# Performance work log

Hardware: AMD Instinct MI355X
Metric: run time of the kernel (lower is better)

Reference implementation:

```python
import jax, jax.numpy as jnp
import numpy as np

N = 50000   # nodes
E = 1600000 # edges
F = 128     # node feature dim
D_ENC, D_EMB, D_H = 32, 12, 128
TEMPERATURE = 10.0


def _dense(key, fan_in, fan_out):
    kw, kb = jax.random.split(key)
    W = jax.random.normal(kw, (fan_in, fan_out), jnp.float32) * (1.0 / jnp.sqrt(fan_in))
    b = jnp.zeros((fan_out,), jnp.float32)
    return W, b


def setup_inputs() -> dict:
    key = jax.random.key(0)
    ks = jax.random.split(key, 12)
    nodes = jax.random.normal(ks[0], (N, F), jnp.float32)
    senders = jax.random.randint(ks[1], (E,), 0, N, dtype=jnp.int32)
    receivers = jax.random.randint(ks[2], (E,), 0, N, dtype=jnp.int32)
    W_enc, b_enc = _dense(ks[3], F, D_ENC)
    W_inf, b_inf = _dense(ks[4], D_ENC + 1, 1)
    W_emb, b_emb = _dense(ks[5], F, D_EMB)
    W1, b1 = _dense(ks[6], D_EMB, D_H)
    W2, b2 = _dense(ks[7], D_H, D_H)
    Wy, by = _dense(ks[8], D_H, 1)
    Wx, bx = _dense(ks[9], D_H, 4)
    return {"nodes": nodes, "senders": senders, "receivers": receivers,
            "W_enc": W_enc, "b_enc": b_enc, "W_inf": W_inf, "b_inf": b_inf,
            "W_emb": W_emb, "b_emb": b_emb, "W1": W1, "b1": b1,
            "W2": W2, "b2": b2, "Wy": Wy, "by": by, "Wx": Wx, "bx": bx}


def reference(nodes, senders, receivers, W_enc, b_enc, W_inf, b_inf,
              W_emb, b_emb, W1, b1, W2, b2, Wy, by, Wx, bx):
    n_nodes = nodes.shape[0]
    # EncodeNet: Dense(32) + relu
    vodes = jax.nn.relu(nodes @ W_enc + b_enc)                      # [N, 32]
    # compute_pure_message: gather by senders, scatter-add by receivers
    msg = jax.ops.segment_sum(vodes[senders], receivers, num_segments=n_nodes)
    vodes = vodes + msg                                             # [N, 32]
    # concat last raw node feature
    vodes = jnp.concatenate([vodes, nodes[:, -1:]], axis=1)         # [N, 33]
    # InfluenceNet: Dense(1), softmax over nodes
    influence = vodes @ W_inf + b_inf                               # [N, 1]
    attention = jax.nn.softmax(influence, axis=0)                   # [N, 1]
    # EmbedNet: Dense(12); softmax-weighted pooling over nodes
    emb = nodes @ W_emb + b_emb                                     # [N, 12]
    g = jnp.sum(emb * attention, axis=0)                            # [12]
    # ActNet head
    h = jax.nn.relu(g @ W1 + b1)
    h = jax.nn.relu(h @ W2 + b2)
    value = h @ Wy + by                                             # [1]
    logits = h @ Wx + bx                                            # [4]
    return (logits / TEMPERATURE, value)
```

## Files before the change

### kernel.cpp

```cpp
#include <hip/hip_runtime.h>
#include <hip/hip_bf16.h>


#define NF 128
#define DENC 32
#define DEMB 12
#define DH 128

#define NSLICE 128
#define R_SCAT 16000
#define NRANGE 4

template <int NJ, int LDW>
__device__ __forceinline__ void gemv_rows(
    const float4* __restrict__ x4p, const float* __restrict__ W,
    int jbase, const float* __restrict__ bias, float* acc, float& x_last)
{
#pragma unroll
    for (int j = 0; j < NJ; j++) acc[j] = bias[jbase + j];
#pragma unroll 2
    for (int c = 0; c < 8; c++) {
        float4 xa = x4p[4 * c + 0];
        float4 xb = x4p[4 * c + 1];
        float4 xc = x4p[4 * c + 2];
        float4 xd = x4p[4 * c + 3];
        float xs[16] = {xa.x, xa.y, xa.z, xa.w, xb.x, xb.y, xb.z, xb.w,
                        xc.x, xc.y, xc.z, xc.w, xd.x, xd.y, xd.z, xd.w};
#pragma unroll
        for (int u = 0; u < 16; u++) {
            const int k = 16 * c + u;
#pragma unroll
            for (int j = 0; j < NJ; j++)
                acc[j] = fmaf(xs[u], W[k * LDW + jbase + j], acc[j]);
        }
        if (c == 7) x_last = xd.w;
    }
}

__global__ __launch_bounds__(256) void k1_node(
    const float* __restrict__ nodes,
    const float* __restrict__ W_enc, const float* __restrict__ b_enc,
    const float* __restrict__ W_inf, const float* __restrict__ b_inf,
    const float* __restrict__ W_emb, const float* __restrict__ b_emb,
    float* __restrict__ p, float* __restrict__ inflb, float* __restrict__ embT,
    int n_nodes)
{
    __shared__ float tabp[3][64];
    const int tid  = threadIdx.x;
    const int lane = tid & 63;
    const int wv   = __builtin_amdgcn_readfirstlane(tid >> 6);
    const int node = blockIdx.x * 64 + lane;
    const bool ok  = (node < n_nodes);
    const float4* x4p = ok ? (const float4*)(nodes + (size_t)node * NF)
                           : (const float4*)nodes;

    float x127 = 0.f;
    if (wv == 3) {
        float acc[DEMB];
        gemv_rows<DEMB, DEMB>(x4p, W_emb, 0, b_emb, acc, x127);
        if (ok) {
#pragma unroll
            for (int j = 0; j < DEMB; j++)
                embT[(size_t)j * n_nodes + node] = acc[j];
        }
    } else {
        const int jbase = __builtin_amdgcn_readfirstlane(wv * 11);
        float pp = 0.f;
        if (wv == 2) {
            float acc[10];
            gemv_rows<10, DENC>(x4p, W_enc, jbase, b_enc, acc, x127);
#pragma unroll
            for (int j = 0; j < 10; j++)
                pp += fmaxf(acc[j], 0.f) * W_inf[jbase + j];
        } else {
            float acc[11];
            gemv_rows<11, DENC>(x4p, W_enc, jbase, b_enc, acc, x127);
#pragma unroll
            for (int j = 0; j < 11; j++)
                pp += fmaxf(acc[j], 0.f) * W_inf[jbase + j];
        }
        tabp[wv][lane] = pp;
    }
    __syncthreads();

    if (wv == 0 && ok) {
        float pn = tabp[0][lane] + tabp[1][lane] + tabp[2][lane];
        p[node] = pn;
        inflb[node] = pn + x127 * W_inf[DENC] + b_inf[0];
    }
}

__global__ __launch_bounds__(512) void k2_scatter(
    const int* __restrict__ senders, const int* __restrict__ recvs,
    const float* __restrict__ p, float* __restrict__ rep,
    int n_nodes, int n_edges)
{
    __shared__ float tab[R_SCAT];
    const int slice = blockIdx.x >> 2;
    const int rng_i = blockIdx.x & 3;
    const int e0 = (int)((long long)n_edges * slice / NSLICE);
    const int e1 = (int)((long long)n_edges * (slice + 1) / NSLICE);
    const int lo = rng_i * R_SCAT;
    const int rng = min(R_SCAT, n_nodes - lo);

    float4* tab4 = (float4*)tab;
    for (int i = threadIdx.x; i < (rng + 3) / 4; i += 512)
        tab4[i] = make_float4(0.f, 0.f, 0.f, 0.f);
    __syncthreads();

    const int ae0 = (e0 + 3) & ~3;
    const int ae1 = e1 & ~3;
    for (int e = e0 + (int)threadIdx.x; e < ae0; e += 512) {
        int r = recvs[e];
        unsigned rr = (unsigned)(r - lo);
        if (rr < (unsigned)rng) atomicAdd(&tab[rr], p[senders[e]]);
    }
    const int4* r4 = (const int4*)recvs;
    const int4* s4 = (const int4*)senders;
    for (int i = ae0 / 4 + (int)threadIdx.x; i < ae1 / 4; i += 512) {
        int4 r = r4[i];
        int4 s = s4[i];
        unsigned rr;
        rr = (unsigned)(r.x - lo); if (rr < (unsigned)rng) atomicAdd(&tab[rr], p[s.x]);
        rr = (unsigned)(r.y - lo); if (rr < (unsigned)rng) atomicAdd(&tab[rr], p[s.y]);
        rr = (unsigned)(r.z - lo); if (rr < (unsigned)rng) atomicAdd(&tab[rr], p[s.z]);
        rr = (unsigned)(r.w - lo); if (rr < (unsigned)rng) atomicAdd(&tab[rr], p[s.w]);
    }
    for (int e = ae1 + (int)threadIdx.x; e < e1; e += 512) {
        int r = recvs[e];
        unsigned rr = (unsigned)(r - lo);
        if (rr < (unsigned)rng) atomicAdd(&tab[rr], p[senders[e]]);
    }
    __syncthreads();

    float* __restrict__ dst = rep + (size_t)slice * n_nodes + lo;
    for (int i = threadIdx.x; i < rng / 4; i += 512)
        ((float4*)dst)[i] = tab4[i];
    for (int i = (rng & ~3) + threadIdx.x; i < rng; i += 512)
        dst[i] = tab[i];
}

__global__ __launch_bounds__(256) void k3_soft(
    const float* __restrict__ inflb, const float* __restrict__ rep,
    const float* __restrict__ embT, float* __restrict__ psum, int n_nodes)
{
    __shared__ float tab[4][64];
    const int tid  = threadIdx.x;
    const int lane = tid & 63;
    const int wv   = __builtin_amdgcn_readfirstlane(tid >> 6);
    const int node = blockIdx.x * 64 + lane;
    const bool ok  = (node < n_nodes);

    float s = 0.f;
    if (ok) {
        const float* r = rep + (size_t)(32 * wv) * n_nodes + node;
#pragma unroll 8
        for (int i = 0; i < NSLICE / 4; i++)
            s += r[(size_t)i * n_nodes];
    }
    tab[wv][lane] = s;
    __syncthreads();

    if (wv == 0) {
        float infl = ok ? inflb[node] + tab[0][lane] + tab[1][lane]
                          + tab[2][lane] + tab[3][lane]
                        : -1e30f;
        float m = infl;
#pragma unroll
        for (int off = 32; off; off >>= 1)
            m = fmaxf(m, __shfl_down(m, off, 64));
        m = __shfl(m, 0, 64);

        const float w = ok ? expf(infl - m) : 0.f;
        float v13[13];
        v13[0] = w;
#pragma unroll
        for (int j = 0; j < DEMB; j++)
            v13[1 + j] = ok ? w * embT[(size_t)j * n_nodes + node] : 0.f;

#pragma unroll
        for (int v = 0; v < 13; v++) {
            float x = v13[v];
#pragma unroll
            for (int off = 32; off; off >>= 1)
                x += __shfl_down(x, off, 64);
            v13[v] = x;
        }
        if (lane == 0) {
            psum[blockIdx.x * 14] = m;
#pragma unroll
            for (int v = 0; v < 13; v++)
                psum[blockIdx.x * 14 + 1 + v] = v13[v];
        }
    }
}

__global__ __launch_bounds__(128) void k4_head(
    const float* __restrict__ psum,
    const float* __restrict__ W1, const float* __restrict__ b1,
    const float* __restrict__ W2, const float* __restrict__ b2,
    const float* __restrict__ Wy, const float* __restrict__ by,
    const float* __restrict__ Wx, const float* __restrict__ bx,
    float* __restrict__ out, int nblk)
{
    const int t = threadIdx.x;
    const int w = t >> 6, l = t & 63;

    float m = -1e30f;
    for (int b = t; b < nblk; b += 128) m = fmaxf(m, psum[b * 14]);
#pragma unroll
    for (int off = 32; off; off >>= 1)
        m = fmaxf(m, __shfl_down(m, off, 64));
    __shared__ float s2[2];
    __shared__ float sM;
    if (l == 0) s2[w] = m;
    __syncthreads();
    if (t == 0) sM = fmaxf(s2[0], s2[1]);
    __syncthreads();
    const float M = sM;

    float acc[13];
#pragma unroll
    for (int v = 0; v < 13; v++) acc[v] = 0.f;
    for (int b = t; b < nblk; b += 128) {
        float sc = expf(psum[b * 14] - M);
#pragma unroll
        for (int v = 0; v < 13; v++)
            acc[v] = fmaf(sc, psum[b * 14 + 1 + v], acc[v]);
    }

    __shared__ float red2[2][13];
#pragma unroll
    for (int v = 0; v < 13; v++) {
        float xx = acc[v];
#pragma unroll
        for (int off = 32; off; off >>= 1)
            xx += __shfl_down(xx, off, 64);
        if (l == 0) red2[w][v] = xx;
    }
    __syncthreads();

    __shared__ float g[DEMB];
    __shared__ float h1[DH];
    __shared__ float h2[DH];
    if (t < DEMB) {
        float S = red2[0][0] + red2[1][0];
        g[t] = (red2[0][1 + t] + red2[1][1 + t]) / S;
    }
    __syncthreads();

    float s1 = b1[t];
#pragma unroll
    for (int i = 0; i < DEMB; i++) s1 = fmaf(g[i], W1[i * DH + t], s1);
    h1[t] = fmaxf(s1, 0.f);
    __syncthreads();

    float s2v = b2[t];
    for (int i = 0; i < DH; i++) s2v = fmaf(h1[i], W2[i * DH + t], s2v);
    h2[t] = fmaxf(s2v, 0.f);
    __syncthreads();

    if (t < 4) {
        float lg = bx[t];
        for (int i = 0; i < DH; i++) lg = fmaf(h2[i], Wx[i * 4 + t], lg);
        out[t] = lg / 10.0f;
    } else if (t == 4) {
        float v = by[0];
        for (int i = 0; i < DH; i++) v = fmaf(h2[i], Wy[i], v);
        out[4] = v;
    }
}

extern "C" void kernel_launch(void* const* d_in, const int* in_sizes, int n_in,
                              void* d_out, int out_size, void* d_ws, size_t ws_size,
                              hipStream_t stream) {
    const float* nodes   = (const float*)d_in[0];
    const int*   senders = (const int*)d_in[1];
    const int*   recvs   = (const int*)d_in[2];
    const float* W_enc   = (const float*)d_in[3];
    const float* b_enc   = (const float*)d_in[4];
    const float* W_inf   = (const float*)d_in[5];
    const float* b_inf   = (const float*)d_in[6];
    const float* W_emb   = (const float*)d_in[7];
    const float* b_emb   = (const float*)d_in[8];
    const float* W1      = (const float*)d_in[9];
    const float* b1      = (const float*)d_in[10];
    const float* W2      = (const float*)d_in[11];
    const float* b2      = (const float*)d_in[12];
    const float* Wy      = (const float*)d_in[13];
    const float* by      = (const float*)d_in[14];
    const float* Wx      = (const float*)d_in[15];
    const float* bx      = (const float*)d_in[16];
    float* out = (float*)d_out;

    const int n_nodes = in_sizes[0] / NF;
    const int n_edges = in_sizes[1];
    const int nb64 = (n_nodes + 63) / 64;

    float* ws    = (float*)d_ws;
    float* p     = ws;
    float* inflb = ws + n_nodes;
    float* embT  = ws + 2 * (size_t)n_nodes;
    float* rep   = ws + 14 * (size_t)n_nodes;
    float* psum  = ws + (14 + NSLICE) * (size_t)n_nodes;

    hipLaunchKernelGGL(k1_node, dim3(nb64), dim3(256), 0, stream,
                       nodes, W_enc, b_enc, W_inf, b_inf, W_emb, b_emb,
                       p, inflb, embT, n_nodes);
    hipLaunchKernelGGL(k2_scatter, dim3(NSLICE * NRANGE), dim3(512), 0, stream,
                       senders, recvs, p, rep, n_nodes, n_edges);
    hipLaunchKernelGGL(k3_soft, dim3(nb64), dim3(256), 0, stream,
                       inflb, rep, embT, psum, n_nodes);
    hipLaunchKernelGGL(k4_head, dim3(1), dim3(128), 0, stream,
                       psum, W1, b1, W2, b2, Wy, by, Wx, bx, out, nb64);
}
```

Baseline: 159.7 us.

## Fuse head into softmax kernel via last-block counter; widen scatter node ranges

The scatter now splits nodes into two ranges of 25000 held in dynamic LDS, with 1024-thread blocks, so each block reads its edge slice twice in total across the grid instead of four times. The separate single-block head kernel is merged into the softmax-pooling kernel: an atomic counter, reset in the first kernel, elects the last finishing block to do the final reduction and MLP. This saves one launch and halves the redundant edge reads, but larger LDS per block may lower occupancy and the last block runs the serial tail.

```diff
diff --git a/kernel.cpp b/kernel.cpp
--- a/kernel.cpp
+++ b/kernel.cpp
@@ -8,8 +8,8 @@
 #define DH 128
 
 #define NSLICE 128
-#define R_SCAT 16000
-#define NRANGE 4
+#define NRANGE 2
+#define R_SCAT 25000
 
 template <int NJ, int LDW>
 __device__ __forceinline__ void gemv_rows(
@@ -43,7 +43,7 @@
     const float* __restrict__ W_inf, const float* __restrict__ b_inf,
     const float* __restrict__ W_emb, const float* __restrict__ b_emb,
     float* __restrict__ p, float* __restrict__ inflb, float* __restrict__ embT,
-    int n_nodes)
+    unsigned* __restrict__ cnt, int n_nodes)
 {
     __shared__ float tabp[3][64];
     const int tid  = threadIdx.x;
@@ -51,6 +51,9 @@
     const int wv   = __builtin_amdgcn_readfirstlane(tid >> 6);
     const int node = blockIdx.x * 64 + lane;
     const bool ok  = (node < n_nodes);
+
+    if (blockIdx.x == 0 && tid == 0) *cnt = 0u;
+
     const float4* x4p = ok ? (const float4*)(nodes + (size_t)node * NF)
                            : (const float4*)nodes;
 
@@ -90,34 +93,33 @@
     }
 }
 
-__global__ __launch_bounds__(512) void k2_scatter(
+__global__ __launch_bounds__(1024) void k2_scatter(
     const int* __restrict__ senders, const int* __restrict__ recvs,
     const float* __restrict__ p, float* __restrict__ rep,
     int n_nodes, int n_edges)
 {
-    __shared__ float tab[R_SCAT];
-    const int slice = blockIdx.x >> 2;
-    const int rng_i = blockIdx.x & 3;
+    extern __shared__ float tab[];
+    const int slice = blockIdx.x >> 1;
+    const int rng_i = blockIdx.x & 1;
     const int e0 = (int)((long long)n_edges * slice / NSLICE);
     const int e1 = (int)((long long)n_edges * (slice + 1) / NSLICE);
     const int lo = rng_i * R_SCAT;
     const int rng = min(R_SCAT, n_nodes - lo);
 
     float4* tab4 = (float4*)tab;
-    for (int i = threadIdx.x; i < (rng + 3) / 4; i += 512)
+    for (int i = threadIdx.x; i < (rng + 3) / 4; i += 1024)
         tab4[i] = make_float4(0.f, 0.f, 0.f, 0.f);
     __syncthreads();
 
     const int ae0 = (e0 + 3) & ~3;
     const int ae1 = e1 & ~3;
-    for (int e = e0 + (int)threadIdx.x; e < ae0; e += 512) {
-        int r = recvs[e];
-        unsigned rr = (unsigned)(r - lo);
+    for (int e = e0 + (int)threadIdx.x; e < ae0; e += 1024) {
+        unsigned rr = (unsigned)(recvs[e] - lo);
         if (rr < (unsigned)rng) atomicAdd(&tab[rr], p[senders[e]]);
     }
     const int4* r4 = (const int4*)recvs;
     const int4* s4 = (const int4*)senders;
-    for (int i = ae0 / 4 + (int)threadIdx.x; i < ae1 / 4; i += 512) {
+    for (int i = ae0 / 4 + (int)threadIdx.x; i < ae1 / 4; i += 1024) {
         int4 r = r4[i];
         int4 s = s4[i];
         unsigned rr;
@@ -126,23 +128,28 @@
         rr = (unsigned)(r.z - lo); if (rr < (unsigned)rng) atomicAdd(&tab[rr], p[s.z]);
         rr = (unsigned)(r.w - lo); if (rr < (unsigned)rng) atomicAdd(&tab[rr], p[s.w]);
     }
-    for (int e = ae1 + (int)threadIdx.x; e < e1; e += 512) {
-        int r = recvs[e];
-        unsigned rr = (unsigned)(r - lo);
+    for (int e = ae1 + (int)threadIdx.x; e < e1; e += 1024) {
+        unsigned rr = (unsigned)(recvs[e] - lo);
         if (rr < (unsigned)rng) atomicAdd(&tab[rr], p[senders[e]]);
     }
     __syncthreads();
 
     float* __restrict__ dst = rep + (size_t)slice * n_nodes + lo;
-    for (int i = threadIdx.x; i < rng / 4; i += 512)
+    for (int i = threadIdx.x; i < rng / 4; i += 1024)
         ((float4*)dst)[i] = tab4[i];
-    for (int i = (rng & ~3) + threadIdx.x; i < rng; i += 512)
+    for (int i = (rng & ~3) + threadIdx.x; i < rng; i += 1024)
         dst[i] = tab[i];
 }
 
-__global__ __launch_bounds__(256) void k3_soft(
+__global__ __launch_bounds__(256) void k34_soft(
     const float* __restrict__ inflb, const float* __restrict__ rep,
-    const float* __restrict__ embT, float* __restrict__ psum, int n_nodes)
+    const float* __restrict__ embT, float* __restrict__ psum,
+    unsigned* __restrict__ cnt,
+    const float* __restrict__ W1, const float* __restrict__ b1,
+    const float* __restrict__ W2, const float* __restrict__ b2,
+    const float* __restrict__ Wy, const float* __restrict__ by,
+    const float* __restrict__ Wx, const float* __restrict__ bx,
+    float* __restrict__ out, int n_nodes, int nblk)
 {
     __shared__ float tab[4][64];
     const int tid  = threadIdx.x;
@@ -193,78 +200,85 @@
                 psum[blockIdx.x * 14 + 1 + v] = v13[v];
         }
     }
-}
-
-__global__ __launch_bounds__(128) void k4_head(
-    const float* __restrict__ psum,
-    const float* __restrict__ W1, const float* __restrict__ b1,
-    const float* __restrict__ W2, const float* __restrict__ b2,
-    const float* __restrict__ Wy, const float* __restrict__ by,
-    const float* __restrict__ Wx, const float* __restrict__ bx,
-    float* __restrict__ out, int nblk)
-{
-    const int t = threadIdx.x;
-    const int w = t >> 6, l = t & 63;
+    __syncthreads();
+
+    __shared__ int is_last;
+    if (tid == 0) {
+        __threadfence();
+        unsigned old = atomicAdd(cnt, 1u);
+        is_last = (old == (unsigned)(nblk - 1)) ? 1 : 0;
+    }
+    __syncthreads();
+    if (!is_last) return;
+    __threadfence();
+
+    const int w4 = tid >> 6, l4 = tid & 63;
 
     float m = -1e30f;
-    for (int b = t; b < nblk; b += 128) m = fmaxf(m, psum[b * 14]);
+    for (int b = tid; b < nblk; b += 256) m = fmaxf(m, psum[b * 14]);
 #pragma unroll
     for (int off = 32; off; off >>= 1)
         m = fmaxf(m, __shfl_down(m, off, 64));
-    __shared__ float s2[2];
+    __shared__ float smx[4];
     __shared__ float sM;
-    if (l == 0) s2[w] = m;
-    __syncthreads();
-    if (t == 0) sM = fmaxf(s2[0], s2[1]);
+    if (l4 == 0) smx[w4] = m;
+    __syncthreads();
+    if (tid == 0)
+        sM = fmaxf(fmaxf(smx[0], smx[1]), fmaxf(smx[2], smx[3]));
     __syncthreads();
     const float M = sM;
 
     float acc[13];
 #pragma unroll
     for (int v = 0; v < 13; v++) acc[v] = 0.f;
-    for (int b = t; b < nblk; b += 128) {
+    for (int b = tid; b < nblk; b += 256) {
         float sc = expf(psum[b * 14] - M);
 #pragma unroll
         for (int v = 0; v < 13; v++)
             acc[v] = fmaf(sc, psum[b * 14 + 1 + v], acc[v]);
     }
 
-    __shared__ float red2[2][13];
+    __shared__ float red[4][13];
 #pragma unroll
     for (int v = 0; v < 13; v++) {
         float xx = acc[v];
 #pragma unroll
         for (int off = 32; off; off >>= 1)
             xx += __shfl_down(xx, off, 64);
-        if (l == 0) red2[w][v] = xx;
+        if (l4 == 0) red[w4][v] = xx;
     }
     __syncthreads();
 
     __shared__ float g[DEMB];
     __shared__ float h1[DH];
     __shared__ float h2[DH];
-    if (t < DEMB) {
-        float S = red2[0][0] + red2[1][0];
-        g[t] = (red2[0][1 + t] + red2[1][1 + t]) / S;
-    }
-    __syncthreads();
-
-    float s1 = b1[t];
-#pragma unroll
-    for (int i = 0; i < DEMB; i++) s1 = fmaf(g[i], W1[i * DH + t], s1);
-    h1[t] = fmaxf(s1, 0.f);
-    __syncthreads();
-
-    float s2v = b2[t];
-    for (int i = 0; i < DH; i++) s2v = fmaf(h1[i], W2[i * DH + t], s2v);
-    h2[t] = fmaxf(s2v, 0.f);
-    __syncthreads();
-
-    if (t < 4) {
-        float lg = bx[t];
-        for (int i = 0; i < DH; i++) lg = fmaf(h2[i], Wx[i * 4 + t], lg);
-        out[t] = lg / 10.0f;
-    } else if (t == 4) {
+    if (tid < DEMB) {
+        float S = red[0][0] + red[1][0] + red[2][0] + red[3][0];
+        g[tid] = (red[0][1 + tid] + red[1][1 + tid] +
+                  red[2][1 + tid] + red[3][1 + tid]) / S;
+    }
+    __syncthreads();
+
+    if (tid < DH) {
+        float s1 = b1[tid];
+#pragma unroll
+        for (int i = 0; i < DEMB; i++) s1 = fmaf(g[i], W1[i * DH + tid], s1);
+        h1[tid] = fmaxf(s1, 0.f);
+    }
+    __syncthreads();
+
+    if (tid < DH) {
+        float s2v = b2[tid];
+        for (int i = 0; i < DH; i++) s2v = fmaf(h1[i], W2[i * DH + tid], s2v);
+        h2[tid] = fmaxf(s2v, 0.f);
+    }
+    __syncthreads();
+
+    if (tid < 4) {
+        float lg = bx[tid];
+        for (int i = 0; i < DH; i++) lg = fmaf(h2[i], Wx[i * 4 + tid], lg);
+        out[tid] = lg / 10.0f;
+    } else if (tid == 4) {
         float v = by[0];
         for (int i = 0; i < DH; i++) v = fmaf(h2[i], Wy[i], v);
         out[4] = v;
@@ -303,14 +317,19 @@
     float* embT  = ws + 2 * (size_t)n_nodes;
     float* rep   = ws + 14 * (size_t)n_nodes;
     float* psum  = ws + (14 + NSLICE) * (size_t)n_nodes;
+    unsigned* cnt = (unsigned*)(psum + (size_t)nb64 * 14 + 4);
+
+    (void)hipFuncSetAttribute((const void*)k2_scatter,
+                              hipFuncAttributeMaxDynamicSharedMemorySize,
+                              R_SCAT * (int)sizeof(float));
 
     hipLaunchKernelGGL(k1_node, dim3(nb64), dim3(256), 0, stream,
                        nodes, W_enc, b_enc, W_inf, b_inf, W_emb, b_emb,
-                       p, inflb, embT, n_nodes);
-    hipLaunchKernelGGL(k2_scatter, dim3(NSLICE * NRANGE), dim3(512), 0, stream,
+                       p, inflb, embT, cnt, n_nodes);
+    hipLaunchKernelGGL(k2_scatter, dim3(NSLICE * NRANGE), dim3(1024),
+                       R_SCAT * sizeof(float), stream,
                        senders, recvs, p, rep, n_nodes, n_edges);
-    hipLaunchKernelGGL(k3_soft, dim3(nb64), dim3(256), 0, stream,
-                       inflb, rep, embT, psum, n_nodes);
-    hipLaunchKernelGGL(k4_head, dim3(1), dim3(128), 0, stream,
-                       psum, W1, b1, W2, b2, Wy, by, Wx, bx, out, nb64);
-}
+    hipLaunchKernelGGL(k34_soft, dim3(nb64), dim3(256), 0, stream,
+                       inflb, rep, embT, psum, cnt,
+                       W1, b1, W2, b2, Wy, by, Wx, bx, out, n_nodes, nb64);
+}
```

Result: slower. 174.1 us (+9.0%).
